# Kernel tuning notes

Hardware: AMD Instinct MI355X
Metric: run time of the kernel (lower is better)

## Reference

```python
import jax, jax.numpy as jnp
import numpy as np

N = 100000   # total nodes in batch
E = 200000   # total edges
G = 4000     # number of graphs
H = 128      # gin_size = gin_hidden = gin_mlp_hidden = linear_hidden
L = 2        # gin_layers


def setup_inputs() -> dict:
    key = jax.random.key(0)
    ks = jax.random.split(key, 24)
    rn = lambda i, shape, s=0.05: (jax.random.normal(ks[i], shape, jnp.float32) * s)
    inp = dict(
        x=rn(0, (N, 14), 1.0),
        edge_attr=rn(1, (E, 4), 1.0),
        edge_index=jax.random.randint(ks[2], (2, E), 0, N, dtype=jnp.int32),
        batch=jnp.sort(jax.random.randint(ks[3], (N,), 0, G, dtype=jnp.int32)),
        node_w=rn(4, (14, H)), node_b=jnp.zeros((H,), jnp.float32),
        edge_w=rn(5, (4, H)), edge_b=jnp.zeros((H,), jnp.float32),
        eps=jnp.zeros((L,), jnp.float32),
        gin_w1=rn(6, (L, H, H)), gin_b1=jnp.zeros((L, H), jnp.float32),
        gin_w2=rn(7, (L, H, H)), gin_b2=jnp.zeros((L, H), jnp.float32),
        em_w1=rn(8, (L, H, H)), em_b1=jnp.zeros((L, H), jnp.float32),
        em_w2=rn(9, (L, H, H)), em_b2=jnp.zeros((L, H), jnp.float32),
        gru_wih=rn(10, (3 * H, H)), gru_whh=rn(11, (3 * H, H)),
        gru_bih=jnp.zeros((3 * H,), jnp.float32), gru_bhh=jnp.zeros((3 * H,), jnp.float32),
        lstm_wih=rn(12, (4 * H, 2 * H)), lstm_whh=rn(13, (4 * H, H)),
        lstm_bih=jnp.zeros((4 * H,), jnp.float32), lstm_bhh=jnp.zeros((4 * H,), jnp.float32),
        fc_w1=rn(14, (2 * H, H)), fc_b1=jnp.zeros((H,), jnp.float32),
        fc_w2=rn(15, (H, 1)), fc_b2=jnp.zeros((1,), jnp.float32),
    )
    return inp


def reference(x, edge_attr, edge_index, batch,
              node_w, node_b, edge_w, edge_b, eps,
              gin_w1, gin_b1, gin_w2, gin_b2,
              em_w1, em_b1, em_w2, em_b2,
              gru_wih, gru_whh, gru_bih, gru_bhh,
              lstm_wih, lstm_whh, lstm_bih, lstm_bhh,
              fc_w1, fc_b1, fc_w2, fc_b2):
    src, dst = edge_index[0], edge_index[1]
    node = x @ node_w + node_b          # [N,H]
    edge = edge_attr @ edge_w + edge_b  # [E,H]
    h = node                            # GRU hidden state
    for l in range(L):
        # GINEConv: msg = relu(x_src + e), scatter-add to dst, (1+eps)*x + agg, then MLP
        msg = jax.nn.relu(node[src] + edge)                     # [E,H] gather
        agg = jax.ops.segment_sum(msg, dst, num_segments=N)     # [N,H] scatter-add
        z = (1.0 + eps[l]) * node + agg
        m = jax.nn.relu(z @ gin_w1[l] + gin_b1[l]) @ gin_w2[l] + gin_b2[l]
        # GRU cell (seq_len=1)
        gi = m @ gru_wih.T + gru_bih
        gh = h @ gru_whh.T + gru_bhh
        ir, iz, inn = jnp.split(gi, 3, axis=-1)
        hr, hz, hn = jnp.split(gh, 3, axis=-1)
        r = jax.nn.sigmoid(ir + hr)
        zt = jax.nn.sigmoid(iz + hz)
        n = jnp.tanh(inn + r * hn)
        h = (1.0 - zt) * n + zt * h
        node = h
        # edge feature update MLP
        edge = jax.nn.relu(edge @ em_w1[l] + em_b1[l]) @ em_w2[l] + em_b2[l]
    # Set2Set pooling, processing_steps=3
    qs = jnp.zeros((G, 2 * H), node.dtype)
    hl = jnp.zeros((G, H), node.dtype)
    cl = jnp.zeros((G, H), node.dtype)
    for _ in range(3):
        g = qs @ lstm_wih.T + lstm_bih + hl @ lstm_whh.T + lstm_bhh
        i_, f_, g_, o_ = jnp.split(g, 4, axis=-1)
        cl = jax.nn.sigmoid(f_) * cl + jax.nn.sigmoid(i_) * jnp.tanh(g_)
        hl = jax.nn.sigmoid(o_) * jnp.tanh(cl)
        q = hl                                                   # [G,H]
        e = jnp.sum(node * q[batch], axis=-1)                    # [N]
        emax = jax.ops.segment_max(e, batch, num_segments=G)
        ex = jnp.exp(e - emax[batch])
        denom = jax.ops.segment_sum(ex, batch, num_segments=G)
        a = ex / jnp.maximum(denom, 1e-9)[batch]                 # per-graph softmax
        r = jax.ops.segment_sum(a[:, None] * node, batch, num_segments=G)  # [G,H]
        qs = jnp.concatenate([q, r], axis=-1)                    # [G,2H]
    out = jax.nn.relu(qs @ fc_w1 + fc_b1) @ fc_w2 + fc_b2
    return out.reshape(-1)
```

## Files before the change

### kernel.cpp

```cpp
#include <hip/hip_runtime.h>
#include <hip/hip_bf16.h>

constexpr int TN = 100000;
constexpr int TE = 200000;
constexpr int TG = 4000;
constexpr int TH = 128;

using short8 = __attribute__((ext_vector_type(8))) short;
using f32x4  = __attribute__((ext_vector_type(4))) float;
typedef __hip_bfloat16 bf16;

#define DEVINL __device__ __forceinline__
DEVINL float sigm(float x)  { return 1.f / (1.f + __expf(-x)); }
DEVINL float ftanh(float x) { return 1.f - 2.f / (__expf(2.f * x) + 1.f); }
DEVINL void unpack8(uint4 v, float* f) {
    const ushort* u = (const ushort*)&v;
#pragma unroll
    for (int j = 0; j < 8; ++j) f[j] = __bfloat162float(*(const bf16*)&u[j]);
}

__global__ void convAll(const float* __restrict__ g1, const float* __restrict__ g2,
                        const float* __restrict__ e1, const float* __restrict__ e2,
                        const float* __restrict__ gwih, const float* __restrict__ gwhh,
                        const float* __restrict__ lwih, const float* __restrict__ lwhh,
                        bf16* __restrict__ w6, bf16* __restrict__ wgru,
                        bf16* __restrict__ wl) {
    int i = blockIdx.x * 256 + threadIdx.x;
    if (i < 6 * TH * TH) {
        int m = i >> 14, r = i & 16383;
        int n = r >> 7, k = r & 127;
        const float* s = (m == 0) ? g1 : (m == 1) ? g1 + TH * TH
                       : (m == 2) ? g2 : (m == 3) ? g2 + TH * TH
                       : (m == 4) ? e1 : e2;
        w6[i] = __float2bfloat16(s[k * TH + n]);
        return;
    }
    i -= 6 * TH * TH;
    if (i < 2 * 384 * TH) {
        const float* s = (i < 384 * TH) ? gwih : gwhh;
        int r = (i < 384 * TH) ? i : i - 384 * TH;
        wgru[i] = __float2bfloat16(s[r]);
        return;
    }
    i -= 2 * 384 * TH;
    if (i < 512 * 256) {
        int c = i >> 8, k = i & 255;
        float v = (k < 128) ? lwih[c * 256 + k] + lwhh[c * 128 + k] : lwih[c * 256 + k];
        wl[i] = __float2bfloat16(v);
    }
}

template<int K>
__global__ __launch_bounds__(256) void proj64(const float* __restrict__ X,
                                              const float* __restrict__ W,
                                              const float* __restrict__ b,
                                              ushort* __restrict__ out, int M) {
    __shared__ float xs[64][K];
    int tid = threadIdx.x;
    int bm = blockIdx.x * 64;
    for (int i = tid; i < 64 * K; i += 256) {
        int r = i / K, k = i % K;
        xs[r][k] = (bm + r < M) ? X[(size_t)(bm + r) * K + k] : 0.f;
    }
    __syncthreads();
    int rb = tid >> 4, h0 = (tid & 15) * 8;
    float acc[4][8];
#pragma unroll
    for (int j = 0; j < 4; ++j)
#pragma unroll
        for (int c = 0; c < 8; ++c) acc[j][c] = b[h0 + c];
#pragma unroll
    for (int k = 0; k < K; ++k) {
        float4 w0 = *(const float4*)(W + k * TH + h0);
        float4 w1 = *(const float4*)(W + k * TH + h0 + 4);
#pragma unroll
        for (int j = 0; j < 4; ++j) {
            float xv = xs[rb + 16 * j][k];
            acc[j][0] = fmaf(xv, w0.x, acc[j][0]); acc[j][1] = fmaf(xv, w0.y, acc[j][1]);
            acc[j][2] = fmaf(xv, w0.z, acc[j][2]); acc[j][3] = fmaf(xv, w0.w, acc[j][3]);
            acc[j][4] = fmaf(xv, w1.x, acc[j][4]); acc[j][5] = fmaf(xv, w1.y, acc[j][5]);
            acc[j][6] = fmaf(xv, w1.z, acc[j][6]); acc[j][7] = fmaf(xv, w1.w, acc[j][7]);
        }
    }
#pragma unroll
    for (int j = 0; j < 4; ++j) {
        int row = bm + rb + 16 * j;
        if (row >= M) continue;
        ushort o[8];
#pragma unroll
        for (int c = 0; c < 8; ++c) {
            bf16 v = __float2bfloat16(acc[j][c]);
            o[c] = *(ushort*)&v;
        }
        *(uint4*)(out + (size_t)row * TH + h0) = *(uint4*)o;
    }
}

__global__ __launch_bounds__(256) void proj_scatter(
    const float* __restrict__ X, const float* __restrict__ W,
    const float* __restrict__ b, const int* __restrict__ perm,
    ushort* __restrict__ out, int M) {
    __shared__ float xs[64][4];
    int tid = threadIdx.x;
    int bm = blockIdx.x * 64;
    if (tid < 64) {
        float4 a = make_float4(0.f, 0.f, 0.f, 0.f);
        if (bm + tid < M) a = *(const float4*)(X + (size_t)(bm + tid) * 4);
        xs[tid][0] = a.x; xs[tid][1] = a.y; xs[tid][2] = a.z; xs[tid][3] = a.w;
    }
    __syncthreads();
    int rb = tid >> 4, h0 = (tid & 15) * 8;
    float acc[4][8];
#pragma unroll
    for (int j = 0; j < 4; ++j)
#pragma unroll
        for (int c = 0; c < 8; ++c) acc[j][c] = b[h0 + c];
#pragma unroll
    for (int k = 0; k < 4; ++k) {
        float4 w0 = *(const float4*)(W + k * TH + h0);
        float4 w1 = *(const float4*)(W + k * TH + h0 + 4);
#pragma unroll
        for (int j = 0; j < 4; ++j) {
            float xv = xs[rb + 16 * j][k];
            acc[j][0] = fmaf(xv, w0.x, acc[j][0]); acc[j][1] = fmaf(xv, w0.y, acc[j][1]);
            acc[j][2] = fmaf(xv, w0.z, acc[j][2]); acc[j][3] = fmaf(xv, w0.w, acc[j][3]);
            acc[j][4] = fmaf(xv, w1.x, acc[j][4]); acc[j][5] = fmaf(xv, w1.y, acc[j][5]);
            acc[j][6] = fmaf(xv, w1.z, acc[j][6]); acc[j][7] = fmaf(xv, w1.w, acc[j][7]);
        }
    }
#pragma unroll
    for (int j = 0; j < 4; ++j) {
        int row = bm + rb + 16 * j;
        if (row >= M) continue;
        ushort o[8];
#pragma unroll
        for (int c = 0; c < 8; ++c) {
            bf16 v = __float2bfloat16(acc[j][c]);
            o[c] = *(ushort*)&v;
        }
        *(uint4*)(out + (size_t)perm[row] * TH + h0) = *(uint4*)o;
    }
}

__global__ void count_deg(const int* __restrict__ ei_dst, int* __restrict__ deg, int En) {
    int e = blockIdx.x * 256 + threadIdx.x;
    if (e < En) atomicAdd(&deg[ei_dst[e]], 1);
}
__global__ void scan_block(const int* __restrict__ deg, int* __restrict__ rowptr,
                           int* __restrict__ bsum, int Nn) {
    __shared__ int sm[256];
    int tid = threadIdx.x;
    int gid = blockIdx.x * 256 + tid;
    int v = (gid < Nn) ? deg[gid] : 0;
    int x = v;
    sm[tid] = x; __syncthreads();
    for (int off = 1; off < 256; off <<= 1) {
        int t = (tid >= off) ? sm[tid - off] : 0;
        __syncthreads();
        x += t; sm[tid] = x;
        __syncthreads();
    }
    if (gid < Nn) rowptr[gid] = x - v;
    if (tid == 255) bsum[blockIdx.x] = x;
}
__global__ void scan_bsum(const int* __restrict__ bsum, int* __restrict__ bsumx, int nb) {
    __shared__ int sm[512];
    int tid = threadIdx.x;
    int v = (tid < nb) ? bsum[tid] : 0;
    int x = v;
    sm[tid] = x; __syncthreads();
    for (int off = 1; off < 512; off <<= 1) {
        int t = (tid >= off) ? sm[tid - off] : 0;
        __syncthreads();
        x += t; sm[tid] = x;
        __syncthreads();
    }
    if (tid < nb) bsumx[tid] = x - v;
}
__global__ void add_off(int* __restrict__ rowptr, const int* __restrict__ bsumx,
                        int Nn, int Etot) {
    int gid = blockIdx.x * 256 + threadIdx.x;
    if (gid < Nn) rowptr[gid] += bsumx[gid >> 8];
    if (gid == 0) rowptr[Nn] = Etot;
}
__global__ void fill_csr(const int* __restrict__ ei_src, const int* __restrict__ ei_dst,
                         const int* __restrict__ rowptr, int* __restrict__ cur,
                         int* __restrict__ srcp, int* __restrict__ epos, int En) {
    int e = blockIdx.x * 256 + threadIdx.x;
    if (e >= En) return;
    int d = ei_dst[e];
    int p = atomicAdd(&cur[d], 1);
    int slot = rowptr[d] + p;
    srcp[slot] = ei_src[e];
    epos[e] = slot;
}
__global__ void build_gptr(const int* __restrict__ batch, int* __restrict__ gptr,
                           int Nn, int Gn) {
    int n = blockIdx.x * 256 + threadIdx.x;
    if (n >= Nn) return;
    int bc = batch[n];
    int bp = (n == 0) ? -1 : batch[n - 1];
    for (int g = bp + 1; g <= bc; ++g) gptr[g] = n;
    if (n == Nn - 1) for (int g = bc + 1; g <= Gn; ++g) gptr[g] = Nn;
}

__global__ __launch_bounds__(256) void aggregate_v8(
    const ushort* __restrict__ node, const ushort* __restrict__ ef,
    const int* __restrict__ srcp, const int* __restrict__ rowptr,
    const float* __restrict__ eps, int l, ushort* __restrict__ zb, int Nn) {
    int t = blockIdx.x * 256 + threadIdx.x;
    int n = t >> 4;
    if (n >= Nn) return;
    int c8 = (t & 15) * 8;
    float se = 1.f + eps[l];
    float acc[8];
    uint4 nv = *(const uint4*)(node + (size_t)n * TH + c8);
    unpack8(nv, acc);
#pragma unroll
    for (int j = 0; j < 8; ++j) acc[j] *= se;
    int s0 = rowptr[n], s1 = rowptr[n + 1];
    int i = s0;
    for (; i + 1 < s1; i += 2) {
        int sa = srcp[i], sb = srcp[i + 1];
        uint4 av0 = *(const uint4*)(node + (size_t)sa * TH + c8);
        uint4 bv0 = *(const uint4*)(ef + (size_t)i * TH + c8);
        uint4 av1 = *(const uint4*)(node + (size_t)sb * TH + c8);
        uint4 bv1 = *(const uint4*)(ef + (size_t)(i + 1) * TH + c8);
        float a0[8], b0[8], a1[8], b1[8];
        unpack8(av0, a0); unpack8(bv0, b0);
        unpack8(av1, a1); unpack8(bv1, b1);
#pragma unroll
        for (int j = 0; j < 8; ++j)
            acc[j] += fmaxf(a0[j] + b0[j], 0.f) + fmaxf(a1[j] + b1[j], 0.f);
    }
    if (i < s1) {
        int sa = srcp[i];
        uint4 av = *(const uint4*)(node + (size_t)sa * TH + c8);
        uint4 bv = *(const uint4*)(ef + (size_t)i * TH + c8);
        float af[8], bf[8];
        unpack8(av, af); unpack8(bv, bf);
#pragma unroll
        for (int j = 0; j < 8; ++j) acc[j] += fmaxf(af[j] + bf[j], 0.f);
    }
    ushort o[8];
#pragma unroll
    for (int j = 0; j < 8; ++j) {
        bf16 v = __float2bfloat16(acc[j]);
        o[j] = *(ushort*)&v;
    }
    *(uint4*)(zb + (size_t)n * TH + c8) = *(uint4*)o;
}

__global__ __launch_bounds__(256) void mlp2_fused(
    const ushort* __restrict__ A, const ushort* __restrict__ W1t,
    const float* __restrict__ b1, const ushort* __restrict__ W2t,
    const float* __restrict__ b2, ushort* __restrict__ C, int M)
{
    __shared__ ushort As[128 * 128];
    __shared__ ushort Ts[128 * 128];
    const int tid = threadIdx.x;
    const int bm = blockIdx.x * 128;
    const int lane = tid & 63, w = tid >> 6;
    const int lr = lane & 15, lq = lane >> 4;
    const int wm = (w & 1) * 64, wn = (w >> 1) * 64;
    short8 wf[4][4];
#pragma unroll
    for (int ni = 0; ni < 4; ++ni)
#pragma unroll
        for (int ks = 0; ks < 4; ++ks)
            wf[ni][ks] = *(const short8*)(W1t + (size_t)(wn + ni * 16 + lr) * 128 + ks * 32 + lq * 8);
#pragma unroll
    for (int p = 0; p < 8; ++p) {
        int ch = p * 256 + tid;
        int r = ch >> 4, c = ch & 15;
        int row = bm + r;
        uint4 v = make_uint4(0u, 0u, 0u, 0u);
        if (row < M) v = *(const uint4*)(A + (size_t)row * 128 + c * 8);
        *(uint4*)(&As[r * 128 + ((c ^ (r & 15)) * 8)]) = v;
    }
    __syncthreads();
    {
        f32x4 acc[4][4] = {};
#pragma unroll
        for (int ks = 0; ks < 4; ++ks) {
            int cb = ks * 4 + lq;
            short8 af[4];
#pragma unroll
            for (int mi = 0; mi < 4; ++mi)
                af[mi] = *(const short8*)(&As[(wm + mi * 16 + lr) * 128 + ((cb ^ lr) * 8)]);
#pragma unroll
            for (int mi = 0; mi < 4; ++mi)
#pragma unroll
                for (int ni = 0; ni < 4; ++ni)
                    acc[mi][ni] = __builtin_amdgcn_mfma_f32_16x16x32_bf16(af[mi], wf[ni][ks], acc[mi][ni], 0, 0, 0);
        }
#pragma unroll
        for (int mi = 0; mi < 4; ++mi)
#pragma unroll
            for (int reg = 0; reg < 4; ++reg) {
                int row = wm + mi * 16 + lq * 4 + reg;
#pragma unroll
                for (int ni = 0; ni < 4; ++ni) {
                    int col = wn + ni * 16 + lr;
                    float v = fmaxf(acc[mi][ni][reg] + b1[col], 0.f);
                    bf16 bv = __float2bfloat16(v);
                    Ts[row * 128 + (((col >> 3) ^ (row & 15)) * 8) + (col & 7)] = *(ushort*)&bv;
                }
            }
    }
#pragma unroll
    for (int ni = 0; ni < 4; ++ni)
#pragma unroll
        for (int ks = 0; ks < 4; ++ks)
            wf[ni][ks] = *(const short8*)(W2t + (size_t)(wn + ni * 16 + lr) * 128 + ks * 32 + lq * 8);
    __syncthreads();
    {
        f32x4 acc[4][4] = {};
#pragma unroll
        for (int ks = 0; ks < 4; ++ks) {
            int cb = ks * 4 + lq;
            short8 af[4];
#pragma unroll
            for (int mi = 0; mi < 4; ++mi)
                af[mi] = *(const short8*)(&Ts[(wm + mi * 16 + lr) * 128 + ((cb ^ lr) * 8)]);
#pragma unroll
            for (int mi = 0; mi < 4; ++mi)
#pragma unroll
                for (int ni = 0; ni < 4; ++ni)
                    acc[mi][ni] = __builtin_amdgcn_mfma_f32_16x16x32_bf16(af[mi], wf[ni][ks], acc[mi][ni], 0, 0, 0);
        }
#pragma unroll
        for (int mi = 0; mi < 4; ++mi)
#pragma unroll
            for (int reg = 0; reg < 4; ++reg) {
                int row = bm + wm + mi * 16 + lq * 4 + reg;
                if (row >= M) continue;
#pragma unroll
                for (int ni = 0; ni < 4; ++ni) {
                    int col = wn + ni * 16 + lr;
                    bf16 bv = __float2bfloat16(acc[mi][ni][reg] + b2[col]);
                    C[(size_t)row * 128 + col] = *(ushort*)&bv;
                }
            }
    }
}

__global__ __launch_bounds__(512, 4) void gru_fused(
    const ushort* __restrict__ mfeat, const ushort* __restrict__ wih,
    const ushort* __restrict__ whh, const float* __restrict__ bih,
    const float* __restrict__ bhh, ushort* __restrict__ node, int Nn)
{
    __shared__ ushort Ms[64 * 128];
    __shared__ ushort Hs[64 * 128];
    const int tid = threadIdx.x;
    const int bm = blockIdx.x * 64;
#pragma unroll
    for (int p = 0; p < 4; ++p) {
        int ch = p * 512 + tid;
        bool isH = ch >= 1024;
        int r = (ch >> 4) & 63, c = ch & 15;
        int row = bm + r;
        uint4 v = make_uint4(0u, 0u, 0u, 0u);
        if (row < Nn) v = *(const uint4*)((isH ? node : mfeat) + (size_t)row * 128 + c * 8);
        ushort* dst = isH ? Hs : Ms;
        *(uint4*)(&dst[r * 128 + ((c ^ (r & 15)) * 8)]) = v;
    }
    __syncthreads();
    const int lane = tid & 63, w = tid >> 6;
    const int lr = lane & 15, lq = lane >> 4;
    const int col = w * 16 + lr;
    f32x4 aR[4] = {}, aZ[4] = {}, aN[4] = {}, aH[4] = {};
#pragma unroll
    for (int ks = 0; ks < 4; ++ks) {
        int koff = ks * 32 + lq * 8;
        short8 wv0 = *(const short8*)(wih + (size_t)col * 128 + koff);
        short8 wv1 = *(const short8*)(wih + (size_t)(128 + col) * 128 + koff);
        short8 wv2 = *(const short8*)(wih + (size_t)(256 + col) * 128 + koff);
        short8 wv3 = *(const short8*)(whh + (size_t)col * 128 + koff);
        short8 wv4 = *(const short8*)(whh + (size_t)(128 + col) * 128 + koff);
        short8 wv5 = *(const short8*)(whh + (size_t)(256 + col) * 128 + koff);
        int cb = ks * 4 + lq;
#pragma unroll
        for (int rt = 0; rt < 4; ++rt) {
            int off = (rt * 16 + lr) * 128 + ((cb ^ lr) * 8);
            short8 am = *(const short8*)(&Ms[off]);
            short8 ah = *(const short8*)(&Hs[off]);
            aR[rt] = __builtin_amdgcn_mfma_f32_16x16x32_bf16(am, wv0, aR[rt], 0, 0, 0);
            aR[rt] = __builtin_amdgcn_mfma_f32_16x16x32_bf16(ah, wv3, aR[rt], 0, 0, 0);
            aZ[rt] = __builtin_amdgcn_mfma_f32_16x16x32_bf16(am, wv1, aZ[rt], 0, 0, 0);
            aZ[rt] = __builtin_amdgcn_mfma_f32_16x16x32_bf16(ah, wv4, aZ[rt], 0, 0, 0);
            aN[rt] = __builtin_amdgcn_mfma_f32_16x16x32_bf16(am, wv2, aN[rt], 0, 0, 0);
            aH[rt] = __builtin_amdgcn_mfma_f32_16x16x32_bf16(ah, wv5, aH[rt], 0, 0, 0);
        }
    }
    {
        int h = col;
        float br = bih[h] + bhh[h];
        float bz = bih[128 + h] + bhh[128 + h];
        float bin = bih[256 + h], bhn = bhh[256 + h];
#pragma unroll
        for (int rt = 0; rt < 4; ++rt)
#pragma unroll
            for (int reg = 0; reg < 4; ++reg) {
                int lrow = rt * 16 + lq * 4 + reg;
                int row = bm + lrow;
                if (row >= Nn) continue;
                float r = sigm(aR[rt][reg] + br);
                float z = sigm(aZ[rt][reg] + bz);
                float n = ftanh(aN[rt][reg] + bin + r * (aH[rt][reg] + bhn));
                int hofs = lrow * 128 + (((h >> 3) ^ (lrow & 15)) * 8) + (h & 7);
                float hold = __bfloat162float(*(const bf16*)&Hs[hofs]);
                bf16 hv = __float2bfloat16((1.f - z) * n + z * hold);
                node[(size_t)row * 128 + h] = *(ushort*)&hv;
            }
    }
}

__global__ __launch_bounds__(256) void lstm_fused(
    ushort* __restrict__ s, const ushort* __restrict__ Wl,
    const float* __restrict__ bih, const float* __restrict__ bhh,
    float* __restrict__ cl, int Gn)
{
    __shared__ ushort Ss[16 * 256];
    const int tid = threadIdx.x;
    const int bm = blockIdx.x * 16;
#pragma unroll
    for (int p = 0; p < 2; ++p) {
        int ch = p * 256 + tid;
        int r = ch >> 5, c = ch & 31;
        int row = bm + r;
        uint4 v = make_uint4(0u, 0u, 0u, 0u);
        if (row < Gn) v = *(const uint4*)(s + (size_t)row * 256 + c * 8);
        *(uint4*)(&Ss[r * 256 + ((c ^ (r & 15)) * 8)]) = v;
    }
    __syncthreads();
    const int lane = tid & 63, w = tid >> 6;
    const int lr = lane & 15, lq = lane >> 4;
    f32x4 acc[4][2] = {};
#pragma unroll
    for (int ks = 0; ks < 8; ++ks) {
        int cb = ks * 4 + lq;
        short8 am = *(const short8*)(&Ss[lr * 256 + ((cb ^ lr) * 8)]);
        int koff = ks * 32 + lq * 8;
#pragma unroll
        for (int g = 0; g < 4; ++g)
#pragma unroll
            for (int sub = 0; sub < 2; ++sub) {
                int col = g * 128 + w * 32 + sub * 16 + lr;
                short8 bf = *(const short8*)(Wl + (size_t)col * 256 + koff);
                acc[g][sub] = __builtin_amdgcn_mfma_f32_16x16x32_bf16(am, bf, acc[g][sub], 0, 0, 0);
            }
    }
#pragma unroll
    for (int sub = 0; sub < 2; ++sub) {
        int h = w * 32 + sub * 16 + lr;
        float bi = bih[h] + bhh[h];
        float bff = bih[128 + h] + bhh[128 + h];
        float bg = bih[256 + h] + bhh[256 + h];
        float bo = bih[384 + h] + bhh[384 + h];
#pragma unroll
        for (int reg = 0; reg < 4; ++reg) {
            int row = bm + lq * 4 + reg;
            if (row >= Gn) continue;
            float iv = sigm(acc[0][sub][reg] + bi);
            float fv = sigm(acc[1][sub][reg] + bff);
            float gv = ftanh(acc[2][sub][reg] + bg);
            float ov = sigm(acc[3][sub][reg] + bo);
            float c = fv * cl[(size_t)row * 128 + h] + iv * gv;
            cl[(size_t)row * 128 + h] = c;
            bf16 hv = __float2bfloat16(ov * ftanh(c));
            s[(size_t)row * 256 + h] = *(ushort*)&hv;
        }
    }
}

__global__ __launch_bounds__(256) void att_fused(
    const ushort* __restrict__ node, ushort* __restrict__ s,
    const int* __restrict__ gptr)
{
    __shared__ float q[128];
    __shared__ float es[512];
    __shared__ float red[8];
    __shared__ float part[16][128];
    int g = blockIdx.x;
    int tid = threadIdx.x, lane = tid & 63, wid = tid >> 6;
    int n0 = gptr[g], n1 = gptr[g + 1];
    int cnt = n1 - n0; if (cnt > 512) cnt = 512;
    if (tid < 128) q[tid] = __bfloat162float(((const bf16*)s)[(size_t)g * 256 + tid]);
    __syncthreads();
    int gr = tid >> 4, c8 = (tid & 15) * 8;
    for (int i0 = 0; i0 < cnt; i0 += 16) {
        int i = i0 + gr;
        float p = 0.f;
        if (i < cnt) {
            uint4 v = *(const uint4*)(node + (size_t)(n0 + i) * TH + c8);
            float f[8]; unpack8(v, f);
#pragma unroll
            for (int j = 0; j < 8; ++j) p = fmaf(f[j], q[c8 + j], p);
        }
        p += __shfl_down(p, 8, 16);
        p += __shfl_down(p, 4, 16);
        p += __shfl_down(p, 2, 16);
        p += __shfl_down(p, 1, 16);
        if ((tid & 15) == 0 && i < cnt) es[i] = p;
    }
    __syncthreads();
    float m = -1e30f;
    for (int i = tid; i < cnt; i += 256) m = fmaxf(m, es[i]);
    for (int off = 32; off; off >>= 1) m = fmaxf(m, __shfl_down(m, off));
    if (lane == 0) red[wid] = m;
    __syncthreads();
    m = fmaxf(fmaxf(red[0], red[1]), fmaxf(red[2], red[3]));
    float sm = 0.f;
    for (int i = tid; i < cnt; i += 256) { float ex = __expf(es[i] - m); es[i] = ex; sm += ex; }
    for (int off = 32; off; off >>= 1) sm += __shfl_down(sm, off);
    if (lane == 0) red[4 + wid] = sm;
    __syncthreads();
    sm = red[4] + red[5] + red[6] + red[7];
    float inv = 1.f / fmaxf(sm, 1e-9f);
    float racc[8] = {};
    for (int i = gr; i < cnt; i += 16) {
        uint4 v = *(const uint4*)(node + (size_t)(n0 + i) * TH + c8);
        float f[8]; unpack8(v, f);
        float a = es[i];
#pragma unroll
        for (int j = 0; j < 8; ++j) racc[j] = fmaf(a, f[j], racc[j]);
    }
#pragma unroll
    for (int j = 0; j < 8; ++j) part[gr][c8 + j] = racc[j];
    __syncthreads();
    if (tid < 128) {
        float r = 0.f;
#pragma unroll
        for (int k = 0; k < 16; ++k) r += part[k][tid];
        bf16 rv = __float2bfloat16(r * inv);
        s[(size_t)g * 256 + 128 + tid] = *(ushort*)&rv;
    }
}

__global__ __launch_bounds__(128) void final_fc(const ushort* __restrict__ s,
                                                const float* __restrict__ w1,
                                                const float* __restrict__ b1,
                                                const float* __restrict__ w2,
                                                const float* __restrict__ b2,
                                                float* __restrict__ out) {
    __shared__ float q[256];
    __shared__ float red[2];
    int g = blockIdx.x, t = threadIdx.x;
    q[t] = __bfloat162float(((const bf16*)s)[(size_t)g * 256 + t]);
    q[t + 128] = __bfloat162float(((const bf16*)s)[(size_t)g * 256 + 128 + t]);
    __syncthreads();
    float acc = b1[t];
    for (int k = 0; k < 256; ++k) acc = fmaf(q[k], w1[k * TH + t], acc);
    acc = fmaxf(acc, 0.f);
    float p = acc * w2[t];
    for (int off = 32; off; off >>= 1) p += __shfl_down(p, off);
    if ((t & 63) == 0) red[t >> 6] = p;
    __syncthreads();
    if (t == 0) out[g] = red[0] + red[1] + b2[0];
}

static void launch_mlp2(const void* A, const bf16* W1t, const float* b1,
                        const bf16* W2t, const float* b2, void* C, int M, hipStream_t s) {
    hipLaunchKernelGGL(mlp2_fused, dim3((M + 127) / 128), dim3(256), 0, s,
                       (const ushort*)A, (const ushort*)W1t, b1, (const ushort*)W2t, b2,
                       (ushort*)C, M);
}

extern "C" void kernel_launch(void* const* d_in, const int* in_sizes, int n_in,
                              void* d_out, int out_size, void* d_ws, size_t ws_size,
                              hipStream_t stream) {
    const float* x         = (const float*)d_in[0];
    const float* edge_attr = (const float*)d_in[1];
    const int*   edge_index= (const int*)d_in[2];
    const int*   batch     = (const int*)d_in[3];
    const float* node_w    = (const float*)d_in[4];
    const float* node_b    = (const float*)d_in[5];
    const float* edge_w    = (const float*)d_in[6];
    const float* edge_b    = (const float*)d_in[7];
    const float* eps       = (const float*)d_in[8];
    const float* gin_w1    = (const float*)d_in[9];
    const float* gin_b1    = (const float*)d_in[10];
    const float* gin_w2    = (const float*)d_in[11];
    const float* gin_b2    = (const float*)d_in[12];
    const float* em_w1     = (const float*)d_in[13];
    const float* em_b1     = (const float*)d_in[14];
    const float* em_w2     = (const float*)d_in[15];
    const float* em_b2     = (const float*)d_in[16];
    const float* gru_wih   = (const float*)d_in[17];
    const float* gru_whh   = (const float*)d_in[18];
    const float* gru_bih   = (const float*)d_in[19];
    const float* gru_bhh   = (const float*)d_in[20];
    const float* lstm_wih  = (const float*)d_in[21];
    const float* lstm_whh  = (const float*)d_in[22];
    const float* lstm_bih  = (const float*)d_in[23];
    const float* lstm_bhh  = (const float*)d_in[24];
    const float* fc_w1     = (const float*)d_in[25];
    const float* fc_b1     = (const float*)d_in[26];
    const float* fc_w2     = (const float*)d_in[27];
    const float* fc_b2     = (const float*)d_in[28];
    float* out = (float*)d_out;
    const int* ei_src = edge_index;
    const int* ei_dst = edge_index + TE;

    char* base = (char*)d_ws;
    size_t off = 0;
    auto alloc = [&](size_t bytes) { void* p = base + off; off += (bytes + 15) & ~size_t(15); return p; };
    bf16*  nodeb = (bf16*)alloc((size_t)TN * TH * 2);
    bf16*  zb    = (bf16*)alloc((size_t)TN * TH * 2);
    bf16*  e1b   = (bf16*)alloc((size_t)TE * TH * 2);
    int*   deg   = (int*)alloc((size_t)TN * 4);
    int*   rowptr= (int*)alloc((size_t)(TN + 1) * 4);
    int*   cur   = (int*)alloc((size_t)TN * 4);
    int*   srcp  = (int*)alloc((size_t)TE * 4);
    int*   epos  = (int*)alloc((size_t)TE * 4);
    int*   bsum  = (int*)alloc(512 * 4);
    int*   bsumx = (int*)alloc(512 * 4);
    int*   gptr  = (int*)alloc((size_t)(TG + 1) * 4);
    bf16*  w6    = (bf16*)alloc(6 * TH * TH * 2);
    bf16*  wgru  = (bf16*)alloc(2 * 384 * TH * 2);
    bf16*  wl    = (bf16*)alloc(512 * 256 * 2);
    if (ws_size < off) return;

    bf16* w_gin1_0 = w6;
    bf16* w_gin1_1 = w6 + 1 * TH * TH;
    bf16* w_gin2_0 = w6 + 2 * TH * TH;
    bf16* w_gin2_1 = w6 + 3 * TH * TH;
    bf16* w_em1    = w6 + 4 * TH * TH;
    bf16* w_em2    = w6 + 5 * TH * TH;
    bf16* w_wih    = wgru;
    bf16* w_whh    = wgru + 384 * TH;

    ushort* sbuf = (ushort*)e1b;
    float*  cl   = (float*)(sbuf + (size_t)TG * 256);

    hipMemsetAsync(deg, 0, (size_t)TN * 4, stream);
    hipMemsetAsync(cur, 0, (size_t)TN * 4, stream);
    count_deg<<<(TE + 255) / 256, 256, 0, stream>>>(ei_dst, deg, TE);
    int nb = (TN + 255) / 256;
    scan_block<<<nb, 256, 0, stream>>>(deg, rowptr, bsum, TN);
    scan_bsum<<<1, 512, 0, stream>>>(bsum, bsumx, nb);
    add_off<<<nb, 256, 0, stream>>>(rowptr, bsumx, TN, TE);
    fill_csr<<<(TE + 255) / 256, 256, 0, stream>>>(ei_src, ei_dst, rowptr, cur, srcp, epos, TE);
    build_gptr<<<(TN + 255) / 256, 256, 0, stream>>>(batch, gptr, TN, TG);

    int convTot = 6 * TH * TH + 2 * 384 * TH + 512 * 256;
    convAll<<<(convTot + 255) / 256, 256, 0, stream>>>(
        gin_w1, gin_w2, em_w1, em_w2, gru_wih, gru_whh, lstm_wih, lstm_whh,
        w6, wgru, wl);

    proj64<14><<<(TN + 63) / 64, 256, 0, stream>>>(x, node_w, node_b, (ushort*)nodeb, TN);
    proj_scatter<<<(TE + 63) / 64, 256, 0, stream>>>(edge_attr, edge_w, edge_b,
                                                     epos, (ushort*)e1b, TE);

    aggregate_v8<<<(TN * 16 + 255) / 256, 256, 0, stream>>>(
        (const ushort*)nodeb, (const ushort*)e1b, srcp, rowptr, eps, 0, (ushort*)zb, TN);
    launch_mlp2(zb, w_gin1_0, gin_b1, w_gin2_0, gin_b2, zb, TN, stream);
    gru_fused<<<(TN + 63) / 64, 512, 0, stream>>>(
        (const ushort*)zb, (const ushort*)w_wih, (const ushort*)w_whh,
        gru_bih, gru_bhh, (ushort*)nodeb, TN);

    launch_mlp2(e1b, w_em1, em_b1, w_em2, em_b2, e1b, TE, stream);
    aggregate_v8<<<(TN * 16 + 255) / 256, 256, 0, stream>>>(
        (const ushort*)nodeb, (const ushort*)e1b, srcp, rowptr, eps, 1, (ushort*)zb, TN);
    launch_mlp2(zb, w_gin1_1, gin_b1 + TH, w_gin2_1, gin_b2 + TH, zb, TN, stream);
    gru_fused<<<(TN + 63) / 64, 512, 0, stream>>>(
        (const ushort*)zb, (const ushort*)w_wih, (const ushort*)w_whh,
        gru_bih, gru_bhh, (ushort*)nodeb, TN);

    hipMemsetAsync(sbuf, 0, (size_t)TG * 256 * 2 + (size_t)TG * 128 * 4, stream);
    for (int st = 0; st < 3; ++st) {
        lstm_fused<<<(TG + 15) / 16, 256, 0, stream>>>(
            sbuf, (const ushort*)wl, lstm_bih, lstm_bhh, cl, TG);
        att_fused<<<TG, 256, 0, stream>>>((const ushort*)nodeb, sbuf, gptr);
    }

    final_fc<<<TG, 128, 0, stream>>>(sbuf, fc_w1, fc_b1, fc_w2, fc_b2, out);
}
```

Baseline: 556.9 us.

## Fuse GIN aggregation into MLP kernel and recompute layer-0 edge features on the fly

The CSR gather-aggregate is merged into the GIN MLP kernel: each block aggregates its 128 nodes straight into shared memory, so the zb round trip and one launch go away. Layer 0 recomputes edge embeddings from edge_attr through an inverse permutation instead of reading a materialized bf16 edge tensor. The edge projection and edge MLP are fused into one edge_pipe kernel. Shared memory is halved by reusing one buffer with an extra barrier, but the aggregation now runs with 8 rows per thread sequentially and an unrolled-by-one neighbor loop, which lowers memory-level parallelism.

```diff
diff --git a/kernel.cpp b/kernel.cpp
--- a/kernel.cpp
+++ b/kernel.cpp
@@ -96,52 +96,6 @@
     }
 }
 
-__global__ __launch_bounds__(256) void proj_scatter(
-    const float* __restrict__ X, const float* __restrict__ W,
-    const float* __restrict__ b, const int* __restrict__ perm,
-    ushort* __restrict__ out, int M) {
-    __shared__ float xs[64][4];
-    int tid = threadIdx.x;
-    int bm = blockIdx.x * 64;
-    if (tid < 64) {
-        float4 a = make_float4(0.f, 0.f, 0.f, 0.f);
-        if (bm + tid < M) a = *(const float4*)(X + (size_t)(bm + tid) * 4);
-        xs[tid][0] = a.x; xs[tid][1] = a.y; xs[tid][2] = a.z; xs[tid][3] = a.w;
-    }
-    __syncthreads();
-    int rb = tid >> 4, h0 = (tid & 15) * 8;
-    float acc[4][8];
-#pragma unroll
-    for (int j = 0; j < 4; ++j)
-#pragma unroll
-        for (int c = 0; c < 8; ++c) acc[j][c] = b[h0 + c];
-#pragma unroll
-    for (int k = 0; k < 4; ++k) {
-        float4 w0 = *(const float4*)(W + k * TH + h0);
-        float4 w1 = *(const float4*)(W + k * TH + h0 + 4);
-#pragma unroll
-        for (int j = 0; j < 4; ++j) {
-            float xv = xs[rb + 16 * j][k];
-            acc[j][0] = fmaf(xv, w0.x, acc[j][0]); acc[j][1] = fmaf(xv, w0.y, acc[j][1]);
-            acc[j][2] = fmaf(xv, w0.z, acc[j][2]); acc[j][3] = fmaf(xv, w0.w, acc[j][3]);
-            acc[j][4] = fmaf(xv, w1.x, acc[j][4]); acc[j][5] = fmaf(xv, w1.y, acc[j][5]);
-            acc[j][6] = fmaf(xv, w1.z, acc[j][6]); acc[j][7] = fmaf(xv, w1.w, acc[j][7]);
-        }
-    }
-#pragma unroll
-    for (int j = 0; j < 4; ++j) {
-        int row = bm + rb + 16 * j;
-        if (row >= M) continue;
-        ushort o[8];
-#pragma unroll
-        for (int c = 0; c < 8; ++c) {
-            bf16 v = __float2bfloat16(acc[j][c]);
-            o[c] = *(ushort*)&v;
-        }
-        *(uint4*)(out + (size_t)perm[row] * TH + h0) = *(uint4*)o;
-    }
-}
-
 __global__ void count_deg(const int* __restrict__ ei_dst, int* __restrict__ deg, int En) {
     int e = blockIdx.x * 256 + threadIdx.x;
     if (e < En) atomicAdd(&deg[ei_dst[e]], 1);
@@ -185,14 +139,14 @@
 }
 __global__ void fill_csr(const int* __restrict__ ei_src, const int* __restrict__ ei_dst,
                          const int* __restrict__ rowptr, int* __restrict__ cur,
-                         int* __restrict__ srcp, int* __restrict__ epos, int En) {
+                         int* __restrict__ srcp, int* __restrict__ einv, int En) {
     int e = blockIdx.x * 256 + threadIdx.x;
     if (e >= En) return;
     int d = ei_dst[e];
     int p = atomicAdd(&cur[d], 1);
     int slot = rowptr[d] + p;
     srcp[slot] = ei_src[e];
-    epos[e] = slot;
+    einv[slot] = e;
 }
 __global__ void build_gptr(const int* __restrict__ batch, int* __restrict__ gptr,
                            int Nn, int Gn) {
@@ -204,62 +158,79 @@
     if (n == Nn - 1) for (int g = bc + 1; g <= Gn; ++g) gptr[g] = Nn;
 }
 
-__global__ __launch_bounds__(256) void aggregate_v8(
+template<bool LAYER0>
+__global__ __launch_bounds__(256) void gin_layer(
     const ushort* __restrict__ node, const ushort* __restrict__ ef,
+    const float* __restrict__ edge_attr, const float* __restrict__ ew,
+    const float* __restrict__ ebp,
     const int* __restrict__ srcp, const int* __restrict__ rowptr,
-    const float* __restrict__ eps, int l, ushort* __restrict__ zb, int Nn) {
-    int t = blockIdx.x * 256 + threadIdx.x;
-    int n = t >> 4;
-    if (n >= Nn) return;
-    int c8 = (t & 15) * 8;
-    float se = 1.f + eps[l];
-    float acc[8];
-    uint4 nv = *(const uint4*)(node + (size_t)n * TH + c8);
-    unpack8(nv, acc);
-#pragma unroll
-    for (int j = 0; j < 8; ++j) acc[j] *= se;
-    int s0 = rowptr[n], s1 = rowptr[n + 1];
-    int i = s0;
-    for (; i + 1 < s1; i += 2) {
-        int sa = srcp[i], sb = srcp[i + 1];
-        uint4 av0 = *(const uint4*)(node + (size_t)sa * TH + c8);
-        uint4 bv0 = *(const uint4*)(ef + (size_t)i * TH + c8);
-        uint4 av1 = *(const uint4*)(node + (size_t)sb * TH + c8);
-        uint4 bv1 = *(const uint4*)(ef + (size_t)(i + 1) * TH + c8);
-        float a0[8], b0[8], a1[8], b1[8];
-        unpack8(av0, a0); unpack8(bv0, b0);
-        unpack8(av1, a1); unpack8(bv1, b1);
-#pragma unroll
-        for (int j = 0; j < 8; ++j)
-            acc[j] += fmaxf(a0[j] + b0[j], 0.f) + fmaxf(a1[j] + b1[j], 0.f);
-    }
-    if (i < s1) {
-        int sa = srcp[i];
-        uint4 av = *(const uint4*)(node + (size_t)sa * TH + c8);
-        uint4 bv = *(const uint4*)(ef + (size_t)i * TH + c8);
-        float af[8], bf[8];
-        unpack8(av, af); unpack8(bv, bf);
-#pragma unroll
-        for (int j = 0; j < 8; ++j) acc[j] += fmaxf(af[j] + bf[j], 0.f);
-    }
-    ushort o[8];
-#pragma unroll
-    for (int j = 0; j < 8; ++j) {
-        bf16 v = __float2bfloat16(acc[j]);
-        o[j] = *(ushort*)&v;
-    }
-    *(uint4*)(zb + (size_t)n * TH + c8) = *(uint4*)o;
-}
-
-__global__ __launch_bounds__(256) void mlp2_fused(
-    const ushort* __restrict__ A, const ushort* __restrict__ W1t,
-    const float* __restrict__ b1, const ushort* __restrict__ W2t,
-    const float* __restrict__ b2, ushort* __restrict__ C, int M)
+    const int* __restrict__ einv, const float* __restrict__ eps, int l,
+    const ushort* __restrict__ W1t, const float* __restrict__ b1,
+    const ushort* __restrict__ W2t, const float* __restrict__ b2,
+    ushort* __restrict__ mout, int M)
 {
     __shared__ ushort As[128 * 128];
-    __shared__ ushort Ts[128 * 128];
     const int tid = threadIdx.x;
     const int bm = blockIdx.x * 128;
+    const int c8 = (tid & 15) * 8;
+    float wz[4][8], ebv[8];
+    if (LAYER0) {
+#pragma unroll
+        for (int k = 0; k < 4; ++k) {
+            float4 w0 = *(const float4*)(ew + k * TH + c8);
+            float4 w1 = *(const float4*)(ew + k * TH + c8 + 4);
+            wz[k][0] = w0.x; wz[k][1] = w0.y; wz[k][2] = w0.z; wz[k][3] = w0.w;
+            wz[k][4] = w1.x; wz[k][5] = w1.y; wz[k][6] = w1.z; wz[k][7] = w1.w;
+        }
+#pragma unroll
+        for (int j = 0; j < 8; ++j) ebv[j] = ebp[c8 + j];
+    }
+    float se = 1.f + eps[l];
+#pragma unroll
+    for (int p = 0; p < 8; ++p) {
+        int r = (tid >> 4) + p * 16;
+        int n = bm + r;
+        ushort o[8] = {0, 0, 0, 0, 0, 0, 0, 0};
+        if (n < M) {
+            float acc[8];
+            uint4 nv = *(const uint4*)(node + (size_t)n * TH + c8);
+            unpack8(nv, acc);
+#pragma unroll
+            for (int j = 0; j < 8; ++j) acc[j] *= se;
+            int s0 = rowptr[n], s1 = rowptr[n + 1];
+            for (int i = s0; i < s1; ++i) {
+                int src = srcp[i];
+                uint4 av = *(const uint4*)(node + (size_t)src * TH + c8);
+                float af[8]; unpack8(av, af);
+                float ev[8];
+                if (LAYER0) {
+                    int e = einv[i];
+                    float4 a = *(const float4*)(edge_attr + (size_t)e * 4);
+#pragma unroll
+                    for (int j = 0; j < 8; ++j) {
+                        float v = ebv[j];
+                        v = fmaf(a.x, wz[0][j], v);
+                        v = fmaf(a.y, wz[1][j], v);
+                        v = fmaf(a.z, wz[2][j], v);
+                        v = fmaf(a.w, wz[3][j], v);
+                        ev[j] = v;
+                    }
+                } else {
+                    uint4 bv = *(const uint4*)(ef + (size_t)i * TH + c8);
+                    unpack8(bv, ev);
+                }
+#pragma unroll
+                for (int j = 0; j < 8; ++j) acc[j] += fmaxf(af[j] + ev[j], 0.f);
+            }
+#pragma unroll
+            for (int j = 0; j < 8; ++j) {
+                bf16 v = __float2bfloat16(acc[j]);
+                o[j] = *(ushort*)&v;
+            }
+        }
+        *(uint4*)(&As[r * 128 + (((c8 >> 3) ^ (r & 15)) * 8)]) = *(uint4*)o;
+    }
+    __syncthreads();
     const int lane = tid & 63, w = tid >> 6;
     const int lr = lane & 15, lq = lane >> 4;
     const int wm = (w & 1) * 64, wn = (w >> 1) * 64;
@@ -269,16 +240,6 @@
 #pragma unroll
         for (int ks = 0; ks < 4; ++ks)
             wf[ni][ks] = *(const short8*)(W1t + (size_t)(wn + ni * 16 + lr) * 128 + ks * 32 + lq * 8);
-#pragma unroll
-    for (int p = 0; p < 8; ++p) {
-        int ch = p * 256 + tid;
-        int r = ch >> 4, c = ch & 15;
-        int row = bm + r;
-        uint4 v = make_uint4(0u, 0u, 0u, 0u);
-        if (row < M) v = *(const uint4*)(A + (size_t)row * 128 + c * 8);
-        *(uint4*)(&As[r * 128 + ((c ^ (r & 15)) * 8)]) = v;
-    }
-    __syncthreads();
     {
         f32x4 acc[4][4] = {};
 #pragma unroll
@@ -294,6 +255,7 @@
                 for (int ni = 0; ni < 4; ++ni)
                     acc[mi][ni] = __builtin_amdgcn_mfma_f32_16x16x32_bf16(af[mi], wf[ni][ks], acc[mi][ni], 0, 0, 0);
         }
+        __syncthreads();
 #pragma unroll
         for (int mi = 0; mi < 4; ++mi)
 #pragma unroll
@@ -304,7 +266,7 @@
                     int col = wn + ni * 16 + lr;
                     float v = fmaxf(acc[mi][ni][reg] + b1[col], 0.f);
                     bf16 bv = __float2bfloat16(v);
-                    Ts[row * 128 + (((col >> 3) ^ (row & 15)) * 8) + (col & 7)] = *(ushort*)&bv;
+                    As[row * 128 + (((col >> 3) ^ (row & 15)) * 8) + (col & 7)] = *(ushort*)&bv;
                 }
             }
     }
@@ -322,7 +284,7 @@
             short8 af[4];
 #pragma unroll
             for (int mi = 0; mi < 4; ++mi)
-                af[mi] = *(const short8*)(&Ts[(wm + mi * 16 + lr) * 128 + ((cb ^ lr) * 8)]);
+                af[mi] = *(const short8*)(&As[(wm + mi * 16 + lr) * 128 + ((cb ^ lr) * 8)]);
 #pragma unroll
             for (int mi = 0; mi < 4; ++mi)
 #pragma unroll
@@ -339,7 +301,126 @@
                 for (int ni = 0; ni < 4; ++ni) {
                     int col = wn + ni * 16 + lr;
                     bf16 bv = __float2bfloat16(acc[mi][ni][reg] + b2[col]);
-                    C[(size_t)row * 128 + col] = *(ushort*)&bv;
+                    mout[(size_t)row * 128 + col] = *(ushort*)&bv;
+                }
+            }
+    }
+}
+
+__global__ __launch_bounds__(256) void edge_pipe(
+    const float* __restrict__ edge_attr, const float* __restrict__ ew,
+    const float* __restrict__ ebp, const int* __restrict__ einv,
+    const ushort* __restrict__ W1t, const float* __restrict__ b1,
+    const ushort* __restrict__ W2t, const float* __restrict__ b2,
+    ushort* __restrict__ e1b, int M)
+{
+    __shared__ ushort As[128 * 128];
+    const int tid = threadIdx.x;
+    const int bm = blockIdx.x * 128;
+    const int c8 = (tid & 15) * 8;
+    float wz[4][8], ebv[8];
+#pragma unroll
+    for (int k = 0; k < 4; ++k) {
+        float4 w0 = *(const float4*)(ew + k * TH + c8);
+        float4 w1 = *(const float4*)(ew + k * TH + c8 + 4);
+        wz[k][0] = w0.x; wz[k][1] = w0.y; wz[k][2] = w0.z; wz[k][3] = w0.w;
+        wz[k][4] = w1.x; wz[k][5] = w1.y; wz[k][6] = w1.z; wz[k][7] = w1.w;
+    }
+#pragma unroll
+    for (int j = 0; j < 8; ++j) ebv[j] = ebp[c8 + j];
+#pragma unroll
+    for (int p = 0; p < 8; ++p) {
+        int r = (tid >> 4) + p * 16;
+        int s = bm + r;
+        ushort o[8] = {0, 0, 0, 0, 0, 0, 0, 0};
+        if (s < M) {
+            int e = einv[s];
+            float4 a = *(const float4*)(edge_attr + (size_t)e * 4);
+#pragma unroll
+            for (int j = 0; j < 8; ++j) {
+                float v = ebv[j];
+                v = fmaf(a.x, wz[0][j], v);
+                v = fmaf(a.y, wz[1][j], v);
+                v = fmaf(a.z, wz[2][j], v);
+                v = fmaf(a.w, wz[3][j], v);
+                bf16 bv = __float2bfloat16(v);
+                o[j] = *(ushort*)&bv;
+            }
+        }
+        *(uint4*)(&As[r * 128 + (((c8 >> 3) ^ (r & 15)) * 8)]) = *(uint4*)o;
+    }
+    __syncthreads();
+    const int lane = tid & 63, w = tid >> 6;
+    const int lr = lane & 15, lq = lane >> 4;
+    const int wm = (w & 1) * 64, wn = (w >> 1) * 64;
+    short8 wf[4][4];
+#pragma unroll
+    for (int ni = 0; ni < 4; ++ni)
+#pragma unroll
+        for (int ks = 0; ks < 4; ++ks)
+            wf[ni][ks] = *(const short8*)(W1t + (size_t)(wn + ni * 16 + lr) * 128 + ks * 32 + lq * 8);
+    {
+        f32x4 acc[4][4] = {};
+#pragma unroll
+        for (int ks = 0; ks < 4; ++ks) {
+            int cb = ks * 4 + lq;
+            short8 af[4];
+#pragma unroll
+            for (int mi = 0; mi < 4; ++mi)
+                af[mi] = *(const short8*)(&As[(wm + mi * 16 + lr) * 128 + ((cb ^ lr) * 8)]);
+#pragma unroll
+            for (int mi = 0; mi < 4; ++mi)
+#pragma unroll
+                for (int ni = 0; ni < 4; ++ni)
+                    acc[mi][ni] = __builtin_amdgcn_mfma_f32_16x16x32_bf16(af[mi], wf[ni][ks], acc[mi][ni], 0, 0, 0);
+        }
+        __syncthreads();
+#pragma unroll
+        for (int mi = 0; mi < 4; ++mi)
+#pragma unroll
+            for (int reg = 0; reg < 4; ++reg) {
+                int row = wm + mi * 16 + lq * 4 + reg;
+#pragma unroll
+                for (int ni = 0; ni < 4; ++ni) {
+                    int col = wn + ni * 16 + lr;
+                    float v = fmaxf(acc[mi][ni][reg] + b1[col], 0.f);
+                    bf16 bv = __float2bfloat16(v);
+                    As[row * 128 + (((col >> 3) ^ (row & 15)) * 8) + (col & 7)] = *(ushort*)&bv;
+                }
+            }
+    }
+#pragma unroll
+    for (int ni = 0; ni < 4; ++ni)
+#pragma unroll
+        for (int ks = 0; ks < 4; ++ks)
+            wf[ni][ks] = *(const short8*)(W2t + (size_t)(wn + ni * 16 + lr) * 128 + ks * 32 + lq * 8);
+    __syncthreads();
+    {
+        f32x4 acc[4][4] = {};
+#pragma unroll
+        for (int ks = 0; ks < 4; ++ks) {
+            int cb = ks * 4 + lq;
+            short8 af[4];
+#pragma unroll
+            for (int mi = 0; mi < 4; ++mi)
+                af[mi] = *(const short8*)(&As[(wm + mi * 16 + lr) * 128 + ((cb ^ lr) * 8)]);
+#pragma unroll
+            for (int mi = 0; mi < 4; ++mi)
+#pragma unroll
+                for (int ni = 0; ni < 4; ++ni)
+                    acc[mi][ni] = __builtin_amdgcn_mfma_f32_16x16x32_bf16(af[mi], wf[ni][ks], acc[mi][ni], 0, 0, 0);
+        }
+#pragma unroll
+        for (int mi = 0; mi < 4; ++mi)
+#pragma unroll
+            for (int reg = 0; reg < 4; ++reg) {
+                int row = bm + wm + mi * 16 + lq * 4 + reg;
+                if (row >= M) continue;
+#pragma unroll
+                for (int ni = 0; ni < 4; ++ni) {
+                    int col = wn + ni * 16 + lr;
+                    bf16 bv = __float2bfloat16(acc[mi][ni][reg] + b2[col]);
+                    e1b[(size_t)row * 128 + col] = *(ushort*)&bv;
                 }
             }
     }
@@ -558,13 +639,6 @@
     if ((t & 63) == 0) red[t >> 6] = p;
     __syncthreads();
     if (t == 0) out[g] = red[0] + red[1] + b2[0];
-}
-
-static void launch_mlp2(const void* A, const bf16* W1t, const float* b1,
-                        const bf16* W2t, const float* b2, void* C, int M, hipStream_t s) {
-    hipLaunchKernelGGL(mlp2_fused, dim3((M + 127) / 128), dim3(256), 0, s,
-                       (const ushort*)A, (const ushort*)W1t, b1, (const ushort*)W2t, b2,
-                       (ushort*)C, M);
 }
 
 extern "C" void kernel_launch(void* const* d_in, const int* in_sizes, int n_in,
@@ -613,7 +687,7 @@
     int*   rowptr= (int*)alloc((size_t)(TN + 1) * 4);
     int*   cur   = (int*)alloc((size_t)TN * 4);
     int*   srcp  = (int*)alloc((size_t)TE * 4);
-    int*   epos  = (int*)alloc((size_t)TE * 4);
+    int*   einv  = (int*)alloc((size_t)TE * 4);
     int*   bsum  = (int*)alloc(512 * 4);
     int*   bsumx = (int*)alloc(512 * 4);
     int*   gptr  = (int*)alloc((size_t)(TG + 1) * 4);
@@ -641,7 +715,7 @@
     scan_block<<<nb, 256, 0, stream>>>(deg, rowptr, bsum, TN);
     scan_bsum<<<1, 512, 0, stream>>>(bsum, bsumx, nb);
     add_off<<<nb, 256, 0, stream>>>(rowptr, bsumx, TN, TE);
-    fill_csr<<<(TE + 255) / 256, 256, 0, stream>>>(ei_src, ei_dst, rowptr, cur, srcp, epos, TE);
+    fill_csr<<<(TE + 255) / 256, 256, 0, stream>>>(ei_src, ei_dst, rowptr, cur, srcp, einv, TE);
     build_gptr<<<(TN + 255) / 256, 256, 0, stream>>>(batch, gptr, TN, TG);
 
     int convTot = 6 * TH * TH + 2 * 384 * TH + 512 * 256;
@@ -650,20 +724,26 @@
         w6, wgru, wl);
 
     proj64<14><<<(TN + 63) / 64, 256, 0, stream>>>(x, node_w, node_b, (ushort*)nodeb, TN);
-    proj_scatter<<<(TE + 63) / 64, 256, 0, stream>>>(edge_attr, edge_w, edge_b,
-                                                     epos, (ushort*)e1b, TE);
-
-    aggregate_v8<<<(TN * 16 + 255) / 256, 256, 0, stream>>>(
-        (const ushort*)nodeb, (const ushort*)e1b, srcp, rowptr, eps, 0, (ushort*)zb, TN);
-    launch_mlp2(zb, w_gin1_0, gin_b1, w_gin2_0, gin_b2, zb, TN, stream);
+
+    gin_layer<true><<<(TN + 127) / 128, 256, 0, stream>>>(
+        (const ushort*)nodeb, nullptr, edge_attr, edge_w, edge_b,
+        srcp, rowptr, einv, eps, 0,
+        (const ushort*)w_gin1_0, gin_b1, (const ushort*)w_gin2_0, gin_b2,
+        (ushort*)zb, TN);
     gru_fused<<<(TN + 63) / 64, 512, 0, stream>>>(
         (const ushort*)zb, (const ushort*)w_wih, (const ushort*)w_whh,
         gru_bih, gru_bhh, (ushort*)nodeb, TN);
 
-    launch_mlp2(e1b, w_em1, em_b1, w_em2, em_b2, e1b, TE, stream);
-    aggregate_v8<<<(TN * 16 + 255) / 256, 256, 0, stream>>>(
-        (const ushort*)nodeb, (const ushort*)e1b, srcp, rowptr, eps, 1, (ushort*)zb, TN);
-    launch_mlp2(zb, w_gin1_1, gin_b1 + TH, w_gin2_1, gin_b2 + TH, zb, TN, stream);
+    edge_pipe<<<(TE + 127) / 128, 256, 0, stream>>>(
+        edge_attr, edge_w, edge_b, einv,
+        (const ushort*)w_em1, em_b1, (const ushort*)w_em2, em_b2,
+        (ushort*)e1b, TE);
+
+    gin_layer<false><<<(TN + 127) / 128, 256, 0, stream>>>(
+        (const ushort*)nodeb, (const ushort*)e1b, nullptr, nullptr, nullptr,
+        srcp, rowptr, einv, eps, 1,
+        (const ushort*)w_gin1_1, gin_b1 + TH, (const ushort*)w_gin2_1, gin_b2 + TH,
+        (ushort*)zb, TN);
     gru_fused<<<(TN + 63) / 64, 512, 0, stream>>>(
         (const ushort*)zb, (const ushort*)w_wih, (const ushort*)w_whh,
         gru_bih, gru_bhh, (ushort*)nodeb, TN);
```

Measured after the change: 603.8 us. 8.4% more time.
